# Kernel tuning notes

Hardware: AMD Instinct MI355X
Metric: run time of the kernel (lower is better)

## Reference

```python
import jax, jax.numpy as jnp
import numpy as np

B, C, H, W = 16, 512, 64, 64
G = 32
CG = C // G       # per-group channels = 16


def setup_inputs() -> dict:
    key = jax.random.key(0)
    ks = jax.random.split(key, 6)
    def w(k, shape, fan_in):
        return (jax.random.normal(k, shape, jnp.float32) / np.float32(np.sqrt(fan_in)))
    return {
        "x": jax.random.normal(ks[0], (B, C, H, W), jnp.float32),
        "conv1_w": w(ks[1], (CG, CG), CG), "conv1_b": jnp.zeros((CG,), jnp.float32),
        "convh_w": w(ks[2], (CG, CG), CG), "convh_b": jnp.zeros((CG,), jnp.float32),
        "convw_w": w(ks[3], (CG, CG), CG), "convw_b": jnp.zeros((CG,), jnp.float32),
        "conv3_w": w(ks[4], (CG, CG, 3, 3), CG * 9), "conv3_b": jnp.zeros((CG,), jnp.float32),
        "gn_w": jnp.ones((CG,), jnp.float32), "gn_b": jnp.zeros((CG,), jnp.float32),
    }


def _conv1x1(y, w, b):
    # y: [N, Ci, L]  w: [Co, Ci]  -> [N, Co, L]
    return jnp.einsum('oi,bil->bol', w, y) + b[None, :, None]


def _ema_forward(x, conv1_w, conv1_b, convh_w, convh_b, convw_w, convw_b,
                 conv3_w, conv3_b, gn_w, gn_b):
    b, c, h, w = x.shape
    g, cg, hw = G, CG, h * w
    bg = b * g
    xg = x.reshape(bg, cg, h, w)

    # coordinate pooling: row means [bg,cg,h], col means [bg,cg,w]
    x_h = xg.mean(axis=3)                     # [bg, cg, h]
    x_w = xg.mean(axis=2)                     # [bg, cg, w]
    y = jnp.concatenate([x_h, x_w], axis=2)   # [bg, cg, h+w]
    y = jax.nn.relu(_conv1x1(y, conv1_w, conv1_b))
    y_h, y_w = y[:, :, :h], y[:, :, h:]

    a_h = jax.nn.sigmoid(_conv1x1(y_h, convh_w, convh_b))[:, :, :, None]  # [bg,cg,h,1]
    a_w = jax.nn.sigmoid(_conv1x1(y_w, convw_w, convw_b))[:, :, None, :]  # [bg,cg,1,w]

    x1 = xg * a_h * a_w

    # GroupNorm(num_groups=1): normalize over (cg,h,w) per sample, affine per channel
    mu = x1.mean(axis=(1, 2, 3), keepdims=True)
    var = ((x1 - mu) ** 2).mean(axis=(1, 2, 3), keepdims=True)
    x2 = (x1 - mu) * jax.lax.rsqrt(var + 1e-5)
    x2 = x2 * gn_w[None, :, None, None] + gn_b[None, :, None, None]

    # 3x3 conv branch
    x3 = jax.lax.conv_general_dilated(
        xg, conv3_w, window_strides=(1, 1), padding='SAME',
        dimension_numbers=('NCHW', 'OIHW', 'NCHW'))
    x3 = jax.nn.relu(x3 + conv3_b[None, :, None, None])

    A2 = jax.nn.softmax(x2.reshape(bg, cg, hw), axis=-1)  # [bg,cg,hw]
    A3 = jax.nn.softmax(x3.reshape(bg, cg, hw), axis=-1)
    V2 = x2.mean(axis=(2, 3))                              # [bg,cg]
    V3 = x3.mean(axis=(2, 3))

    s2 = jnp.einsum('bc,bcl->bl', V2, A3)  # [bg, hw]
    s3 = jnp.einsum('bc,bcl->bl', V3, A2)
    s = jax.nn.softmax(s2 + s3, axis=-1).reshape(bg, 1, h, w)

    return (xg * s).reshape(b, c, h, w)


def reference(x, conv1_w, conv1_b, convh_w, convh_b, convw_w, convw_b,
              conv3_w, conv3_b, gn_w, gn_b):
    return _ema_forward(x, conv1_w, conv1_b, convh_w, convh_b, convw_w, convw_b,
                        conv3_w, conv3_b, gn_w, gn_b)
```

## Files before the change

kernel.cpp:

```cpp
#include <hip/hip_runtime.h>
#include <hip/hip_bf16.h>

#define CHW  65536
#define CHW4 16384
#define KSTR 76

__device__ __forceinline__ float wred(float v){
#pragma unroll
  for (int o = 32; o; o >>= 1) v += __shfl_xor(v, o, 64);
  return v;
}
__device__ __forceinline__ float wred16(float v){
#pragma unroll
  for (int o = 8; o; o >>= 1) v += __shfl_xor(v, o, 64);
  return v;
}
__device__ __forceinline__ float bf2f(unsigned short u){
  return __uint_as_float(((unsigned)u) << 16);
}
__device__ __forceinline__ unsigned short f2b(float f){
  union { __hip_bfloat16 h; unsigned short u; } cv;
  cv.h = __float2bfloat16(f);
  return cv.u;
}

__global__ __launch_bounds__(256, 6) void k3_conv(const float* __restrict__ x,
    const float* __restrict__ w3, const float* __restrict__ b3,
    __hip_bfloat16* __restrict__ E3,
    float* __restrict__ V3part, float* __restrict__ Z3part,
    float* __restrict__ rs_g, float* __restrict__ csp_g)
{
  __shared__ __align__(16) float in_s[8*10*KSTR];
  int tid = threadIdx.x;
  int st  = blockIdx.x;
  int bg  = blockIdx.y;
  size_t base  = (size_t)bg * CHW;
  const float4* x4 = (const float4*)x + (size_t)bg * CHW4;
  int lane = tid & 63;
  int cog = __builtin_amdgcn_readfirstlane(tid >> 6);
  int co0 = cog * 4;
  int r  = lane >> 3;
  int cc = lane & 7;
  float acc[4][8];
#pragma unroll
  for (int i = 0; i < 4; ++i)
#pragma unroll
    for (int px = 0; px < 8; ++px) acc[i][px] = 0.f;

#pragma unroll 1
  for (int half = 0; half < 2; ++half){
    __syncthreads();
    for (int idx = tid; idx < 1440; idx += 256){
      int p   = idx % 18;
      int rr  = (idx / 18) % 10;
      int ci8 = idx / 180;
      int sl  = (p <= 8) ? 2*p : 2*(p-9)+1;
      int hh  = st*8 - 1 + rr;
      float4 v = make_float4(0.f, 0.f, 0.f, 0.f);
      if (sl >= 1 && sl <= 16 && (unsigned)hh < 64u)
        v = x4[(half*8 + ci8)*1024 + hh*16 + (sl-1)];
      *(float4*)&in_s[(ci8*10 + rr)*KSTR + p*4] = v;
    }
    __syncthreads();

    {
      int task = tid >> 2, sub = tid & 3;
      int pci = task >> 3, prow = task & 7;
      const float* rowp = &in_s[(pci*10 + 1 + prow)*KSTR];
      float4 a  = *(const float4*)(rowp + 4*(2*sub+9));
      float4 b  = *(const float4*)(rowp + 4*(2*sub+1));
      float4 cf = *(const float4*)(rowp + 4*(2*sub+10));
      float4 d  = *(const float4*)(rowp + 4*(2*sub+2));
      float sm = a.x+a.y+a.z+a.w + b.x+b.y+b.z+b.w
               + cf.x+cf.y+cf.z+cf.w + d.x+d.y+d.z+d.w;
      sm += __shfl_xor(sm, 1, 64);
      sm += __shfl_xor(sm, 2, 64);
      if (sub == 0)
        rs_g[(size_t)bg*1024 + (half*8 + pci)*64 + st*8 + prow] = sm;
    }
    {
      int pci = tid >> 5;
      int c0  = (tid & 31) * 2;
#pragma unroll
      for (int e = 0; e < 2; ++e){
        int c  = c0 + e;
        int sl = (c >> 2) + 1;
        int pp = (sl >> 1) + 9*(sl & 1);
        int dd = pp*4 + (c & 3);
        float a2 = 0.f;
#pragma unroll
        for (int rr2 = 0; rr2 < 8; ++rr2)
          a2 += in_s[(pci*10 + 1 + rr2)*KSTR + dd];
        csp_g[((size_t)(bg*8 + st)*16 + half*8 + pci)*64 + c] = a2;
      }
    }

#pragma unroll 1
    for (int ci8 = 0; ci8 < 8; ++ci8){
      int ci = half*8 + ci8;
      float wgt[4][9];
#pragma unroll
      for (int i = 0; i < 4; ++i)
#pragma unroll
        for (int t = 0; t < 9; ++t)
          wgt[i][t] = w3[((co0+i)*16 + ci)*9 + t];
#pragma unroll
      for (int dy = 0; dy < 3; ++dy){
        const float* rowp = &in_s[(ci8*10 + r + dy)*KSTR];
        float4 A0  = *(const float4*)(rowp + 4*cc);
        float4 A1  = *(const float4*)(rowp + 4*(cc+9));
        float4 A2v = *(const float4*)(rowp + 4*(cc+1));
        float4 A3v = *(const float4*)(rowp + 4*(cc+10));
        float v[16] = {A0.x,A0.y,A0.z,A0.w, A1.x,A1.y,A1.z,A1.w,
                       A2v.x,A2v.y,A2v.z,A2v.w, A3v.x,A3v.y,A3v.z,A3v.w};
#pragma unroll
        for (int dx = 0; dx < 3; ++dx){
#pragma unroll
          for (int px = 0; px < 8; ++px){
            float iv = v[px + dx + 3];
#pragma unroll
            for (int i = 0; i < 4; ++i)
              acc[i][px] = fmaf(wgt[i][dy*3+dx], iv, acc[i][px]);
          }
        }
      }
    }
  }
  int hh = st*8 + r;
#pragma unroll
  for (int i = 0; i < 4; ++i){
    float bias = b3[co0+i];
    union { unsigned short hb[8]; uint4 u; } pk;
    float v3acc = 0.f, z3acc = 0.f;
#pragma unroll
    for (int px = 0; px < 8; ++px){
      float val = fmaxf(acc[i][px] + bias, 0.f);
      float e = __expf(val);
      v3acc += val;
      z3acc += e;
      pk.hb[px] = f2b(e);
    }
    *(uint4*)&E3[base + (size_t)(co0+i)*4096 + hh*64 + cc*8] = pk.u;
    float rv = wred(v3acc);
    float rz = wred(z3acc);
    if (lane == 0){
      V3part[((size_t)bg*8 + st)*16 + co0 + i] = rv;
      Z3part[((size_t)bg*8 + st)*16 + co0 + i] = rz;
    }
  }
}

__global__ __launch_bounds__(1024, 8) void mega(const float* __restrict__ x,
    const float* __restrict__ w1, const float* __restrict__ b1,
    const float* __restrict__ wh, const float* __restrict__ bh,
    const float* __restrict__ ww, const float* __restrict__ bw,
    const float* __restrict__ gnw, const float* __restrict__ gnb,
    const float* __restrict__ V3part, const float* __restrict__ Z3part,
    const float* __restrict__ rs_g, const float* __restrict__ csp_g,
    const __hip_bfloat16* __restrict__ E3,
    float* __restrict__ out)
{
  __shared__ float rs[1024];
  __shared__ float cs[1024];
  __shared__ float ym[2048];
  __shared__ __align__(16) float ahs[1024], aws[1024];
  __shared__ float chpart[256], zpart[256];
  __shared__ float red1[16], red2[16];
  __shared__ float murs[2];
  __shared__ float sc_s[16], of_s[16], v2_s[16], p2s[16], p3s[16];
  __shared__ float invS_s;

  int tid = threadIdx.x, bg = blockIdx.x;
  const float4* x4 = (const float4*)x + (size_t)bg * CHW4;
  const ushort4* E34 = (const ushort4*)E3 + (size_t)bg * CHW4;
  float4* o4 = (float4*)out + (size_t)bg * CHW4;
  int h = tid >> 4, w4 = tid & 15, lane = tid & 63, wv = tid >> 6;

  rs[tid] = rs_g[(size_t)bg*1024 + tid];
  {
    const float* cp = csp_g + (size_t)bg*8192;
    float csum = 0.f;
#pragma unroll
    for (int ss = 0; ss < 8; ++ss) csum += cp[ss*1024 + tid];
    cs[tid] = csum;
  }
  __syncthreads();
  for (int ol = tid; ol < 2048; ol += 1024){
    int o = ol >> 7, l = ol & 127;
    float acc = b1[o];
#pragma unroll
    for (int i = 0; i < 16; ++i){
      float mv = (l < 64 ? rs[i*64 + l] : cs[i*64 + (l-64)]) * (1.f/64.f);
      acc = fmaf(w1[o*16 + i], mv, acc);
    }
    ym[o*128 + l] = fmaxf(acc, 0.f);
  }
  __syncthreads();
  for (int ol = tid; ol < 2048; ol += 1024){
    int q = ol >> 10;
    int o = (ol >> 6) & 15;
    int p = ol & 63;
    const float* Wm = q ? ww : wh;
    float acc = q ? bw[o] : bh[o];
#pragma unroll
    for (int i = 0; i < 16; ++i)
      acc = fmaf(Wm[o*16 + i], ym[i*128 + q*64 + p], acc);
    float sg = 1.f / (1.f + __expf(-acc));
    (q ? aws : ahs)[o*64 + p] = sg;
  }
  __syncthreads();

  const float4* aws4 = (const float4*)aws;
  float s1 = 0.f, s2 = 0.f;
#pragma unroll 4
  for (int k = 0; k < 16; ++k){
    float4 v = x4[k*1024 + tid];
    float ah = ahs[k*64 + h];
    float4 aw = aws4[k*16 + w4];
    float4 x1;
    x1.x = v.x * ah * aw.x;
    x1.y = v.y * ah * aw.y;
    x1.z = v.z * ah * aw.z;
    x1.w = v.w * ah * aw.w;
    float csum = x1.x + x1.y + x1.z + x1.w;
    s1 += csum;
    s2 = fmaf(x1.x, x1.x, s2); s2 = fmaf(x1.y, x1.y, s2);
    s2 = fmaf(x1.z, x1.z, s2); s2 = fmaf(x1.w, x1.w, s2);
    float cw = wred(csum);
    if (lane == 0) chpart[k*16 + wv] = cw;
  }
  float r1 = wred(s1), r2 = wred(s2);
  if (lane == 0){ red1[wv] = r1; red2[wv] = r2; }
  __syncthreads();
  if (tid == 0){
    float S = 0.f, SS = 0.f;
#pragma unroll
    for (int i = 0; i < 16; ++i){ S += red1[i]; SS += red2[i]; }
    float mu = S * (1.f/65536.f);
    float var = SS * (1.f/65536.f) - mu*mu;
    murs[0] = mu; murs[1] = rsqrtf(var + 1e-5f);
  }
  __syncthreads();
  if (tid < 16){
    float ch = 0.f;
#pragma unroll
    for (int m = 0; m < 16; ++m) ch += chpart[tid*16 + m];
    float mu = murs[0], rstd = murs[1];
    float g = gnw[tid], b = gnb[tid];
    float sc = rstd * g;
    sc_s[tid] = sc; of_s[tid] = b - mu*sc;
    v2_s[tid] = (ch * (1.f/4096.f) - mu) * sc + b;
  }
  __syncthreads();

  unsigned e2a[16], e2b[16];
#pragma unroll 2
  for (int k = 0; k < 16; ++k){
    float4 v = x4[k*1024 + tid];
    float ah = ahs[k*64 + h];
    float4 aw = aws4[k*16 + w4];
    float sc = sc_s[k], of = of_s[k];
    float ex = __expf(fmaf(v.x * ah * aw.x, sc, of));
    float ey = __expf(fmaf(v.y * ah * aw.y, sc, of));
    float ez = __expf(fmaf(v.z * ah * aw.z, sc, of));
    float ew = __expf(fmaf(v.w * ah * aw.w, sc, of));
    float z = ex + ey + ez + ew;
    e2a[k] = (unsigned)f2b(ex) | ((unsigned)f2b(ey) << 16);
    e2b[k] = (unsigned)f2b(ez) | ((unsigned)f2b(ew) << 16);
    float zw = wred(z);
    if (lane == 0) zpart[k*16 + wv] = zw;
  }
  __syncthreads();
  if (tid < 16){
    float z2 = 0.f;
#pragma unroll
    for (int m = 0; m < 16; ++m) z2 += zpart[tid*16 + m];
    float v3 = 0.f, z3 = 0.f;
#pragma unroll
    for (int ss = 0; ss < 8; ++ss){
      v3 += V3part[((size_t)bg*8 + ss)*16 + tid];
      z3 += Z3part[((size_t)bg*8 + ss)*16 + tid];
    }
    p2s[tid] = v3 * (1.f/4096.f) / z2;
    p3s[tid] = v2_s[tid] / z3;
  }
  __syncthreads();

  float4 tacc = make_float4(0.f,0.f,0.f,0.f);
#pragma unroll 4
  for (int k = 0; k < 16; ++k){
    ushort4 eu = E34[k*1024 + tid];
    float p2 = p2s[k], p3 = p3s[k];
    tacc.x += bf2f((unsigned short)(e2a[k] & 0xffffu))*p2 + bf2f(eu.x)*p3;
    tacc.y += bf2f((unsigned short)(e2a[k] >> 16))   *p2 + bf2f(eu.y)*p3;
    tacc.z += bf2f((unsigned short)(e2b[k] & 0xffffu))*p2 + bf2f(eu.z)*p3;
    tacc.w += bf2f((unsigned short)(e2b[k] >> 16))   *p2 + bf2f(eu.w)*p3;
  }
  float4 e;
  e.x = __expf(tacc.x); e.y = __expf(tacc.y);
  e.z = __expf(tacc.z); e.w = __expf(tacc.w);
  float es = e.x + e.y + e.z + e.w;
  float rr = wred(es);
  if (lane == 0) red1[wv] = rr;
  __syncthreads();
  if (tid == 0){
    float S = 0.f;
#pragma unroll
    for (int i = 0; i < 16; ++i) S += red1[i];
    invS_s = 1.f / S;
  }
  __syncthreads();
  float iS = invS_s;
  float4 ei = make_float4(e.x*iS, e.y*iS, e.z*iS, e.w*iS);

#pragma unroll 4
  for (int k = 0; k < 16; ++k){
    float4 v = x4[k*1024 + tid];
    float4 ov;
    ov.x = v.x * ei.x; ov.y = v.y * ei.y;
    ov.z = v.z * ei.z; ov.w = v.w * ei.w;
    o4[k*1024 + tid] = ov;
  }
}

extern "C" void kernel_launch(void* const* d_in, const int* in_sizes, int n_in,
                              void* d_out, int out_size, void* d_ws, size_t ws_size,
                              hipStream_t stream)
{
  const float* x   = (const float*)d_in[0];
  const float* w1  = (const float*)d_in[1];
  const float* b1  = (const float*)d_in[2];
  const float* wh  = (const float*)d_in[3];
  const float* bh  = (const float*)d_in[4];
  const float* ww  = (const float*)d_in[5];
  const float* bw  = (const float*)d_in[6];
  const float* w3  = (const float*)d_in[7];
  const float* b3  = (const float*)d_in[8];
  const float* gnw = (const float*)d_in[9];
  const float* gnb = (const float*)d_in[10];
  float* out = (float*)d_out;

  float* V3part = (float*)d_ws;
  float* Z3part = V3part + 65536;
  float* rs_g   = Z3part + 65536;
  float* csp_g  = rs_g + 524288;
  __hip_bfloat16* E3 = (__hip_bfloat16*)(csp_g + 4194304);
  (void)ws_size; (void)n_in; (void)in_sizes; (void)out_size;

  k3_conv<<<dim3(8, 512), 256, 0, stream>>>(x, w3, b3, E3, V3part, Z3part,
                                            rs_g, csp_g);
  mega   <<<512, 1024, 0, stream>>>(x, w1, b1, wh, bh, ww, bw, gnw, gnb,
                                    V3part, Z3part, rs_g, csp_g, E3, out);
}
```

Measured before the change: 446.2 us.

## Load conv inputs directly from global memory instead of staging through LDS

The 3x3 conv kernel drops the shared-memory tile and its two barriers per half. Each thread now loads its own 3-row by 4-float4 neighbourhood straight from global memory for every input channel and relies on cache for the halo reuse. The row and column pooling partials are recomputed from registers with wave shuffles, with the work spread across waves by channel. This removes LDS traffic and synchronisation but issues redundant global loads per wave and lowers the occupancy hint from 6 to 5.

```diff
diff --git a/kernel.cpp b/kernel.cpp
--- a/kernel.cpp
+++ b/kernel.cpp
@@ -3,16 +3,10 @@
 
 #define CHW  65536
 #define CHW4 16384
-#define KSTR 76
 
 __device__ __forceinline__ float wred(float v){
 #pragma unroll
   for (int o = 32; o; o >>= 1) v += __shfl_xor(v, o, 64);
-  return v;
-}
-__device__ __forceinline__ float wred16(float v){
-#pragma unroll
-  for (int o = 8; o; o >>= 1) v += __shfl_xor(v, o, 64);
   return v;
 }
 __device__ __forceinline__ float bf2f(unsigned short u){
@@ -24,13 +18,12 @@
   return cv.u;
 }
 
-__global__ __launch_bounds__(256, 6) void k3_conv(const float* __restrict__ x,
+__global__ __launch_bounds__(256, 5) void k3_conv(const float* __restrict__ x,
     const float* __restrict__ w3, const float* __restrict__ b3,
     __hip_bfloat16* __restrict__ E3,
     float* __restrict__ V3part, float* __restrict__ Z3part,
     float* __restrict__ rs_g, float* __restrict__ csp_g)
 {
-  __shared__ __align__(16) float in_s[8*10*KSTR];
   int tid = threadIdx.x;
   int st  = blockIdx.x;
   int bg  = blockIdx.y;
@@ -41,92 +34,76 @@
   int co0 = cog * 4;
   int r  = lane >> 3;
   int cc = lane & 7;
+  int h0 = st*8 + r;
+  int sl0 = cc*2;
+
   float acc[4][8];
 #pragma unroll
   for (int i = 0; i < 4; ++i)
 #pragma unroll
     for (int px = 0; px < 8; ++px) acc[i][px] = 0.f;
 
+  const float4 z4 = make_float4(0.f, 0.f, 0.f, 0.f);
+
 #pragma unroll 1
-  for (int half = 0; half < 2; ++half){
-    __syncthreads();
-    for (int idx = tid; idx < 1440; idx += 256){
-      int p   = idx % 18;
-      int rr  = (idx / 18) % 10;
-      int ci8 = idx / 180;
-      int sl  = (p <= 8) ? 2*p : 2*(p-9)+1;
-      int hh  = st*8 - 1 + rr;
-      float4 v = make_float4(0.f, 0.f, 0.f, 0.f);
-      if (sl >= 1 && sl <= 16 && (unsigned)hh < 64u)
-        v = x4[(half*8 + ci8)*1024 + hh*16 + (sl-1)];
-      *(float4*)&in_s[(ci8*10 + rr)*KSTR + p*4] = v;
-    }
-    __syncthreads();
-
-    {
-      int task = tid >> 2, sub = tid & 3;
-      int pci = task >> 3, prow = task & 7;
-      const float* rowp = &in_s[(pci*10 + 1 + prow)*KSTR];
-      float4 a  = *(const float4*)(rowp + 4*(2*sub+9));
-      float4 b  = *(const float4*)(rowp + 4*(2*sub+1));
-      float4 cf = *(const float4*)(rowp + 4*(2*sub+10));
-      float4 d  = *(const float4*)(rowp + 4*(2*sub+2));
-      float sm = a.x+a.y+a.z+a.w + b.x+b.y+b.z+b.w
-               + cf.x+cf.y+cf.z+cf.w + d.x+d.y+d.z+d.w;
+  for (int ci = 0; ci < 16; ++ci){
+    float4 R[3][4];
+#pragma unroll
+    for (int dy = 0; dy < 3; ++dy){
+      int hh = h0 - 1 + dy;
+      bool rok = (unsigned)hh < 64u;
+      const float4* rp = &x4[ci*1024 + hh*16];
+      R[dy][0] = (rok && cc > 0) ? rp[sl0-1] : z4;
+      R[dy][1] = rok ? rp[sl0]   : z4;
+      R[dy][2] = rok ? rp[sl0+1] : z4;
+      R[dy][3] = (rok && cc < 7) ? rp[sl0+2] : z4;
+    }
+    float wgt[4][9];
+#pragma unroll
+    for (int i = 0; i < 4; ++i)
+#pragma unroll
+      for (int t = 0; t < 9; ++t)
+        wgt[i][t] = w3[((co0+i)*16 + ci)*9 + t];
+#pragma unroll
+    for (int dy = 0; dy < 3; ++dy){
+      float v[16] = {R[dy][0].x,R[dy][0].y,R[dy][0].z,R[dy][0].w,
+                     R[dy][1].x,R[dy][1].y,R[dy][1].z,R[dy][1].w,
+                     R[dy][2].x,R[dy][2].y,R[dy][2].z,R[dy][2].w,
+                     R[dy][3].x,R[dy][3].y,R[dy][3].z,R[dy][3].w};
+#pragma unroll
+      for (int dx = 0; dx < 3; ++dx){
+#pragma unroll
+        for (int px = 0; px < 8; ++px){
+          float iv = v[px + dx + 3];
+#pragma unroll
+          for (int i = 0; i < 4; ++i)
+            acc[i][px] = fmaf(wgt[i][dy*3+dx], iv, acc[i][px]);
+        }
+      }
+    }
+    if (cog == (ci & 3)){
+      float sm = R[1][1].x+R[1][1].y+R[1][1].z+R[1][1].w
+               + R[1][2].x+R[1][2].y+R[1][2].z+R[1][2].w;
       sm += __shfl_xor(sm, 1, 64);
       sm += __shfl_xor(sm, 2, 64);
-      if (sub == 0)
-        rs_g[(size_t)bg*1024 + (half*8 + pci)*64 + st*8 + prow] = sm;
-    }
-    {
-      int pci = tid >> 5;
-      int c0  = (tid & 31) * 2;
-#pragma unroll
-      for (int e = 0; e < 2; ++e){
-        int c  = c0 + e;
-        int sl = (c >> 2) + 1;
-        int pp = (sl >> 1) + 9*(sl & 1);
-        int dd = pp*4 + (c & 3);
-        float a2 = 0.f;
-#pragma unroll
-        for (int rr2 = 0; rr2 < 8; ++rr2)
-          a2 += in_s[(pci*10 + 1 + rr2)*KSTR + dd];
-        csp_g[((size_t)(bg*8 + st)*16 + half*8 + pci)*64 + c] = a2;
+      sm += __shfl_xor(sm, 4, 64);
+      if (cc == 0) rs_g[(size_t)bg*1024 + ci*64 + h0] = sm;
+      float4 ca = R[1][1], cb = R[1][2];
+#pragma unroll
+      for (int o = 8; o < 64; o <<= 1){
+        ca.x += __shfl_xor(ca.x, o, 64); ca.y += __shfl_xor(ca.y, o, 64);
+        ca.z += __shfl_xor(ca.z, o, 64); ca.w += __shfl_xor(ca.w, o, 64);
+        cb.x += __shfl_xor(cb.x, o, 64); cb.y += __shfl_xor(cb.y, o, 64);
+        cb.z += __shfl_xor(cb.z, o, 64); cb.w += __shfl_xor(cb.w, o, 64);
       }
-    }
-
-#pragma unroll 1
-    for (int ci8 = 0; ci8 < 8; ++ci8){
-      int ci = half*8 + ci8;
-      float wgt[4][9];
-#pragma unroll
-      for (int i = 0; i < 4; ++i)
-#pragma unroll
-        for (int t = 0; t < 9; ++t)
-          wgt[i][t] = w3[((co0+i)*16 + ci)*9 + t];
-#pragma unroll
-      for (int dy = 0; dy < 3; ++dy){
-        const float* rowp = &in_s[(ci8*10 + r + dy)*KSTR];
-        float4 A0  = *(const float4*)(rowp + 4*cc);
-        float4 A1  = *(const float4*)(rowp + 4*(cc+9));
-        float4 A2v = *(const float4*)(rowp + 4*(cc+1));
-        float4 A3v = *(const float4*)(rowp + 4*(cc+10));
-        float v[16] = {A0.x,A0.y,A0.z,A0.w, A1.x,A1.y,A1.z,A1.w,
-                       A2v.x,A2v.y,A2v.z,A2v.w, A3v.x,A3v.y,A3v.z,A3v.w};
-#pragma unroll
-        for (int dx = 0; dx < 3; ++dx){
-#pragma unroll
-          for (int px = 0; px < 8; ++px){
-            float iv = v[px + dx + 3];
-#pragma unroll
-            for (int i = 0; i < 4; ++i)
-              acc[i][px] = fmaf(wgt[i][dy*3+dx], iv, acc[i][px]);
-          }
-        }
+      if (r == 0){
+        float* cp = &csp_g[((size_t)(bg*8 + st)*16 + ci)*64 + cc*8];
+        *(float4*)&cp[0] = ca;
+        *(float4*)&cp[4] = cb;
       }
     }
   }
-  int hh = st*8 + r;
+
 #pragma unroll
   for (int i = 0; i < 4; ++i){
     float bias = b3[co0+i];
@@ -140,7 +117,7 @@
       z3acc += e;
       pk.hb[px] = f2b(e);
     }
-    *(uint4*)&E3[base + (size_t)(co0+i)*4096 + hh*64 + cc*8] = pk.u;
+    *(uint4*)&E3[base + (size_t)(co0+i)*4096 + h0*64 + cc*8] = pk.u;
     float rv = wred(v3acc);
     float rz = wred(z3acc);
     if (lane == 0){
```

Measured after the change: 1.230 ms. 176% more time.
